# Kernel tuning notes

Measured on AMD Instinct MI355X. Metric: run time of the kernel, lower is better.

## Reference

```python
import jax, jax.numpy as jnp
import numpy as np

N_NODES = 100000

def _spmm(edge_index, edge_weight, support):
    # out[dst] += w * support[src]  == sparse adj @ support
    src, dst = edge_index[0], edge_index[1]
    msgs = support[src] * edge_weight[:, None]
    return jax.ops.segment_sum(msgs, dst, num_segments=N_NODES)


def setup_inputs() -> dict:
    key = jax.random.key(0)
    k1, k2, k3, k4, k5 = jax.random.split(key, 5)
    n_feat, n_hid, n_class = 512, 256, 40
    E = 3200000
    x = jax.random.normal(k1, (N_NODES, n_feat), dtype=jnp.float32)
    edge_index = jax.random.randint(k2, (2, E), 0, N_NODES, dtype=jnp.int64)
    edge_weight = jax.random.uniform(k3, (E,), dtype=jnp.float32)
    # Xavier-uniform-like init
    lim1 = float(np.sqrt(6.0 / (n_feat + n_hid)))
    lim2 = float(np.sqrt(6.0 / (n_hid + n_class)))
    W1 = jax.random.uniform(k4, (n_feat, n_hid), minval=-lim1, maxval=lim1, dtype=jnp.float32)
    W2 = jax.random.uniform(k5, (n_hid, n_class), minval=-lim2, maxval=lim2, dtype=jnp.float32)
    return {"x": x, "edge_index": edge_index, "edge_weight": edge_weight, "W1": W1, "W2": W2}


def reference(x, edge_index, edge_weight, W1, W2):
    # layer 1: dense projection then sparse aggregation, relu
    h = jax.nn.relu(_spmm(edge_index, edge_weight, x @ W1))
    # dropout is identity in eval mode (deterministic reference)
    # layer 2
    logits = _spmm(edge_index, edge_weight, h @ W2)
    return jax.nn.log_softmax(logits, axis=1)
```

## Files before the change

### kernel.cpp

```cpp
#include <hip/hip_runtime.h>
#include <math.h>

#define N_FEAT 512
#define F_HID  256
#define F_OUT  40

#define NBLK1 256
#define CAP   48

typedef unsigned short u16;
typedef unsigned int   u32;
typedef unsigned char  u8;
typedef __attribute__((ext_vector_type(8))) short bf8_t;
typedef __attribute__((ext_vector_type(4))) float f32x4;
typedef __attribute__((ext_vector_type(2))) float f32x2;

__device__ __forceinline__ u16 f2bf(float f) {
    unsigned u = __float_as_uint(f);
    u += 0x7FFFu + ((u >> 16) & 1u);
    return (u16)(u >> 16);
}
__device__ __forceinline__ float bfLo(u32 u) { return __uint_as_float(u << 16); }
__device__ __forceinline__ float bfHi(u32 u) { return __uint_as_float(u & 0xFFFF0000u); }

__global__ void prep_weights(const float* __restrict__ W1, const float* __restrict__ W2,
                             u16* __restrict__ W1T, u16* __restrict__ W2T) {
    int idx = blockIdx.x * blockDim.x + threadIdx.x;
    if (idx < F_HID * N_FEAT) {
        int n = idx >> 9, k = idx & 511;
        W1T[idx] = f2bf(W1[k * F_HID + n]);
    }
    int idx2 = idx - F_HID * N_FEAT;
    if (idx2 >= 0 && idx2 < 48 * 256) {
        int n = idx2 >> 8, k = idx2 & 255;
        W2T[idx2] = (n < F_OUT) ? f2bf(W2[k * F_OUT + n]) : (u16)0;
    }
}

__global__ __launch_bounds__(256) void bucket_kernel(const int* __restrict__ src,
                                                     const int* __restrict__ dst,
                                                     const float* __restrict__ w,
                                                     int2* __restrict__ region,
                                                     int* __restrict__ cnt_g,
                                                     int E, int NB) {
    __shared__ int cnt[1024];
    int tid = threadIdx.x;
    for (int i = tid; i < 1024; i += 256) cnt[i] = 0;
    __syncthreads();
    int2* myreg = region + (size_t)blockIdx.x * NB * CAP;
    for (int i = blockIdx.x * 256 + tid; i < E; i += NBLK1 * 256) {
        int d = dst[i];
        int b = d >> 7;
        int pos = atomicAdd(&cnt[b], 1);
        if (pos < CAP)
            myreg[(size_t)b * CAP + pos] =
                make_int2((d & 127) | (src[i] << 7), __float_as_int(w[i]));
    }
    __syncthreads();
    for (int t = tid; t < NB; t += 256)
        cnt_g[blockIdx.x * NB + t] = min(cnt[t], CAP);
}

__global__ __launch_bounds__(256) void scan_tot(const int* __restrict__ cnt_g,
                                                int* __restrict__ tot, int NB) {
    __shared__ int s[256];
    int b = blockIdx.x, tid = threadIdx.x;
    s[tid] = cnt_g[tid * NB + b];
    __syncthreads();
    for (int d = 128; d > 0; d >>= 1) {
        if (tid < d) s[tid] += s[tid + d];
        __syncthreads();
    }
    if (tid == 0) tot[b] = s[0];
}

__global__ __launch_bounds__(256) void bucket_scan(const int* __restrict__ tot,
                                                   int* __restrict__ Bb, int NB) {
    __shared__ int t4[1024];
    __shared__ int part[256];
    int tid = threadIdx.x;
    for (int i = tid; i < 1024; i += 256) t4[i] = (i < NB) ? tot[i] : 0;
    __syncthreads();
    int loc[4], s = 0;
#pragma unroll
    for (int j = 0; j < 4; ++j) { loc[j] = s; s += t4[tid * 4 + j]; }
    part[tid] = s;
    __syncthreads();
    for (int d = 1; d < 256; d <<= 1) {
        int v = (tid >= d) ? part[tid - d] : 0;
        __syncthreads();
        part[tid] += v;
        __syncthreads();
    }
    int pb = part[tid] - s;
#pragma unroll
    for (int j = 0; j < 4; ++j) {
        int b = tid * 4 + j;
        if (b < NB) Bb[b] = pb + loc[j];
    }
}

__global__ __launch_bounds__(256) void build_csr(const int2* __restrict__ region,
                                                 const int* __restrict__ cnt_g,
                                                 const int* __restrict__ Bb,
                                                 int* __restrict__ deg,
                                                 int* __restrict__ offs,
                                                 int2* __restrict__ edges,
                                                 int M, int NB) {
    int b = blockIdx.x, tid = threadIdx.x;
    __shared__ int hist[128], curi[128], pc[NBLK1], s1[256];
    if (tid < 128) hist[tid] = 0;
    pc[tid] = cnt_g[tid * NB + b];
    __syncthreads();
    int sub = tid >> 4, l = tid & 15;
    for (int bl = sub; bl < NBLK1; bl += 16) {
        int n = pc[bl];
        const int2* rp = region + ((size_t)bl * NB + b) * CAP;
        for (int j = l; j < n; j += 16)
            atomicAdd(&hist[rp[j].x & 127], 1);
    }
    __syncthreads();
    int h = (tid < 128) ? hist[tid] : 0;
    s1[tid] = h;
    __syncthreads();
    for (int dd = 1; dd < 128; dd <<= 1) {
        int v = (tid >= dd) ? s1[tid - dd] : 0;
        __syncthreads();
        s1[tid] += v;
        __syncthreads();
    }
    int base = Bb[b];
    if (tid < 128) {
        int ex = s1[tid] - h;
        curi[tid] = ex;
        int d = b * 128 + tid;
        if (d < M) { deg[d] = h; offs[d] = base + ex; }
    }
    __syncthreads();
    for (int bl = sub; bl < NBLK1; bl += 16) {
        int n = pc[bl];
        const int2* rp = region + ((size_t)bl * NB + b) * CAP;
        for (int j = l; j < n; j += 16) {
            int2 e = rp[j];
            int p = atomicAdd(&curi[e.x & 127], 1);
            edges[base + p] = make_int2(e.x >> 7, e.y);
        }
    }
}

__global__ __launch_bounds__(256) void gemm1_kernel(const float* __restrict__ X,
                                                    const u16* __restrict__ W1T,
                                                    u8* __restrict__ H0, int M) {
    __shared__ float As[2][2048];
    int tid  = threadIdx.x;
    int wv   = tid >> 6, lane = tid & 63;
    int l15  = lane & 15, quad = lane >> 4;
    int m0   = blockIdx.x * 64;

    int p16_0 = wv * 64 + lane;
    int p16_1 = 256 + wv * 64 + lane;
    int r0 = p16_0 >> 3, sc0 = (p16_0 & 7) ^ (r0 & 7);
    int r1 = p16_1 >> 3, sc1 = (p16_1 & 7) ^ (r1 & 7);
    const float* src0 = X + (size_t)min(m0 + r0, M - 1) * N_FEAT + sc0 * 4;
    const float* src1 = X + (size_t)min(m0 + r1, M - 1) * N_FEAT + sc1 * 4;

    f32x4 acc[4][4] = {};

    auto stage = [&](int c, int buf) {
        __builtin_amdgcn_global_load_lds(
            (const __attribute__((address_space(1))) void*)(src0 + c * 32),
            (__attribute__((address_space(3))) void*)(&As[buf][wv * 256]), 16, 0, 0);
        __builtin_amdgcn_global_load_lds(
            (const __attribute__((address_space(1))) void*)(src1 + c * 32),
            (__attribute__((address_space(3))) void*)(&As[buf][1024 + wv * 256]), 16, 0, 0);
    };

    stage(0, 0);
    __syncthreads();
    for (int c = 0; c < 16; ++c) {
        int cur = c & 1;
        if (c + 1 < 16) stage(c + 1, cur ^ 1);
        bf8_t b[4];
#pragma unroll
        for (int nt = 0; nt < 4; ++nt)
            b[nt] = *(const bf8_t*)(W1T + (size_t)(wv * 64 + nt * 16 + l15) * N_FEAT + c * 32 + quad * 8);
#pragma unroll
        for (int mt = 0; mt < 4; ++mt) {
            int m = mt * 16 + l15;
            int scA = (quad * 2) ^ (m & 7);
            int scB = (quad * 2 + 1) ^ (m & 7);
            f32x4 x0 = *(const f32x4*)(&As[cur][m * 32 + scA * 4]);
            f32x4 x1 = *(const f32x4*)(&As[cur][m * 32 + scB * 4]);
            bf8_t a;
            a[0] = (short)f2bf(x0[0]); a[1] = (short)f2bf(x0[1]);
            a[2] = (short)f2bf(x0[2]); a[3] = (short)f2bf(x0[3]);
            a[4] = (short)f2bf(x1[0]); a[5] = (short)f2bf(x1[1]);
            a[6] = (short)f2bf(x1[2]); a[7] = (short)f2bf(x1[3]);
#pragma unroll
            for (int nt = 0; nt < 4; ++nt)
                acc[mt][nt] = __builtin_amdgcn_mfma_f32_16x16x32_bf16(a, b[nt], acc[mt][nt], 0, 0, 0);
        }
        __syncthreads();
    }
#pragma unroll
    for (int mt = 0; mt < 4; ++mt)
#pragma unroll
        for (int nt = 0; nt < 4; ++nt)
#pragma unroll
            for (int r = 0; r < 4; ++r) {
                int row = m0 + mt * 16 + quad * 4 + r;
                if (row < M) {
                    int pk = __builtin_amdgcn_cvt_pk_fp8_f32(acc[mt][nt][r], 0.f, 0, false);
                    H0[(size_t)row * F_HID + wv * 64 + nt * 16 + l15] = (u8)(pk & 0xFF);
                }
            }
}

__global__ __launch_bounds__(256) void spmm1_kernel(const u8* __restrict__ H0,
                                                    const int* __restrict__ offs,
                                                    const int* __restrict__ deg,
                                                    const int2* __restrict__ edges,
                                                    u16* __restrict__ H1, int M) {
    __shared__ int2 sE[4][64];
    int wv = threadIdx.x >> 6, lane = threadIdx.x & 63;
    int d = blockIdx.x * 4 + wv;
    if (d >= M) return;
    int start = offs[d], cnt = deg[d];
    int q = lane >> 4, l16 = lane & 15;
    const u8* hp = H0 + l16 * 16;
    float acc[16] = {};
    for (int base = 0; base < cnt; base += 64) {
        int c = min(64, cnt - base);
        int2 ev = make_int2(0, 0);
        if (lane < c) ev = edges[start + base + lane];
        sE[wv][lane] = ev;
        int jt = (c + 31) >> 5;
        for (int j = 0; j < jt; ++j) {
            int2 e[8];
#pragma unroll
            for (int k = 0; k < 8; ++k)
                e[k] = sE[wv][32 * j + 4 * k + q];
            uint4 v[8];
#pragma unroll
            for (int k = 0; k < 8; ++k)
                v[k] = *(const uint4*)(hp + (size_t)e[k].x * F_HID);
#pragma unroll
            for (int k = 0; k < 8; ++k) {
                if (32 * j + 4 * k < c) {
                    float w = __int_as_float(e[k].y);
                    u32 wd[4] = {v[k].x, v[k].y, v[k].z, v[k].w};
#pragma unroll
                    for (int t = 0; t < 4; ++t) {
                        f32x2 lo = __builtin_amdgcn_cvt_pk_f32_fp8((int)wd[t], false);
                        f32x2 hi = __builtin_amdgcn_cvt_pk_f32_fp8((int)wd[t], true);
                        acc[4 * t + 0] = fmaf(w, lo[0], acc[4 * t + 0]);
                        acc[4 * t + 1] = fmaf(w, lo[1], acc[4 * t + 1]);
                        acc[4 * t + 2] = fmaf(w, hi[0], acc[4 * t + 2]);
                        acc[4 * t + 3] = fmaf(w, hi[1], acc[4 * t + 3]);
                    }
                }
            }
        }
    }
#pragma unroll
    for (int t = 0; t < 16; ++t) {
        acc[t] += __shfl_xor(acc[t], 16);
        acc[t] += __shfl_xor(acc[t], 32);
    }
    if (q == 0) {
        u16 o[16];
#pragma unroll
        for (int t = 0; t < 16; ++t) o[t] = f2bf(fmaxf(acc[t], 0.f));
        uint4 r0, r1;
        r0.x = (u32)o[0]  | ((u32)o[1]  << 16);
        r0.y = (u32)o[2]  | ((u32)o[3]  << 16);
        r0.z = (u32)o[4]  | ((u32)o[5]  << 16);
        r0.w = (u32)o[6]  | ((u32)o[7]  << 16);
        r1.x = (u32)o[8]  | ((u32)o[9]  << 16);
        r1.y = (u32)o[10] | ((u32)o[11] << 16);
        r1.z = (u32)o[12] | ((u32)o[13] << 16);
        r1.w = (u32)o[14] | ((u32)o[15] << 16);
        uint4* dst16 = (uint4*)(H1 + (size_t)d * F_HID + l16 * 16);
        dst16[0] = r0;
        dst16[1] = r1;
    }
}

__global__ __launch_bounds__(256) void gemm2_kernel(const u16* __restrict__ H1,
                                                    const u16* __restrict__ W2T,
                                                    u8* __restrict__ P, int M) {
    __shared__ u16 Bs[2][8192];
    int tid  = threadIdx.x;
    int wv   = tid >> 6, lane = tid & 63;
    int l15  = lane & 15, quad = lane >> 4;
    int m0   = blockIdx.x * 128;

    f32x4 acc[2][3] = {};

    auto stage = [&](int c, int buf) {
#pragma unroll
        for (int jj = 0; jj < 4; ++jj) {
            int p16 = jj * 256 + wv * 64 + lane;
            int r   = p16 >> 3;
            int sc  = (p16 & 7) ^ (r & 7);
            const u16* src = H1 + (size_t)min(m0 + r, M - 1) * F_HID + c * 64 + sc * 8;
            __builtin_amdgcn_global_load_lds(
                (const __attribute__((address_space(1))) void*)src,
                (__attribute__((address_space(3))) void*)(&Bs[buf][jj * 2048 + wv * 512]), 16, 0, 0);
        }
    };

    stage(0, 0);
    __syncthreads();
    for (int c = 0; c < 4; ++c) {
        int cur = c & 1;
        if (c + 1 < 4) stage(c + 1, cur ^ 1);
#pragma unroll
        for (int ks = 0; ks < 2; ++ks) {
            bf8_t b[3];
#pragma unroll
            for (int nt = 0; nt < 3; ++nt)
                b[nt] = *(const bf8_t*)(W2T + (size_t)(nt * 16 + l15) * F_HID + c * 64 + ks * 32 + quad * 8);
#pragma unroll
            for (int mt = 0; mt < 2; ++mt) {
                int m  = wv * 32 + mt * 16 + l15;
                int sc = (ks * 4 + quad) ^ (m & 7);
                bf8_t a = *(const bf8_t*)(&Bs[cur][m * 64 + sc * 8]);
#pragma unroll
                for (int nt = 0; nt < 3; ++nt)
                    acc[mt][nt] = __builtin_amdgcn_mfma_f32_16x16x32_bf16(a, b[nt], acc[mt][nt], 0, 0, 0);
            }
        }
        __syncthreads();
    }
#pragma unroll
    for (int mt = 0; mt < 2; ++mt)
#pragma unroll
        for (int nt = 0; nt < 3; ++nt)
#pragma unroll
            for (int r = 0; r < 4; ++r) {
                int row = m0 + wv * 32 + mt * 16 + quad * 4 + r;
                int col = nt * 16 + l15;
                if (row < M) {
                    u8 val = 0;
                    if (col < F_OUT) {
                        int pk = __builtin_amdgcn_cvt_pk_fp8_f32(acc[mt][nt][r], 0.f, 0, false);
                        val = (u8)(pk & 0xFF);
                    }
                    P[(size_t)row * 64 + col] = val;
                }
            }
    for (int rr = tid; rr < 128; rr += 256) {
        int row = m0 + rr;
        if (row < M) *(uint4*)(P + (size_t)row * 64 + 48) = make_uint4(0, 0, 0, 0);
    }
}

__global__ __launch_bounds__(256) void spmm2_kernel(const u8* __restrict__ P,
                                                    const int* __restrict__ offs,
                                                    const int* __restrict__ deg,
                                                    const int2* __restrict__ edges,
                                                    float* __restrict__ out, int M) {
    __shared__ int2 sE[4][64];
    int wv = threadIdx.x >> 6, lane = threadIdx.x & 63;
    int d = blockIdx.x * 4 + wv;
    if (d >= M) return;
    int start = offs[d], cnt = deg[d];
    int g = lane >> 3, l8 = lane & 7;
    const u8* pp = P + l8 * 8;
    float acc[8] = {};
    for (int base = 0; base < cnt; base += 64) {
        int c = min(64, cnt - base);
        int2 ev = make_int2(0, 0);
        if (lane < c) ev = edges[start + base + lane];
        sE[wv][lane] = ev;
        int2 e[8];
#pragma unroll
        for (int k = 0; k < 8; ++k)
            e[k] = sE[wv][8 * k + g];
        uint2 v[8];
#pragma unroll
        for (int k = 0; k < 8; ++k)
            v[k] = *(const uint2*)(pp + (size_t)e[k].x * 64);
#pragma unroll
        for (int k = 0; k < 8; ++k) {
            if (8 * k < c) {
                float w = __int_as_float(e[k].y);
                f32x2 lo0 = __builtin_amdgcn_cvt_pk_f32_fp8((int)v[k].x, false);
                f32x2 hi0 = __builtin_amdgcn_cvt_pk_f32_fp8((int)v[k].x, true);
                f32x2 lo1 = __builtin_amdgcn_cvt_pk_f32_fp8((int)v[k].y, false);
                f32x2 hi1 = __builtin_amdgcn_cvt_pk_f32_fp8((int)v[k].y, true);
                acc[0] = fmaf(w, lo0[0], acc[0]); acc[1] = fmaf(w, lo0[1], acc[1]);
                acc[2] = fmaf(w, hi0[0], acc[2]); acc[3] = fmaf(w, hi0[1], acc[3]);
                acc[4] = fmaf(w, lo1[0], acc[4]); acc[5] = fmaf(w, lo1[1], acc[5]);
                acc[6] = fmaf(w, hi1[0], acc[6]); acc[7] = fmaf(w, hi1[1], acc[7]);
            }
        }
    }
#pragma unroll
    for (int t = 0; t < 8; ++t) {
        acc[t] += __shfl_xor(acc[t], 8);
        acc[t] += __shfl_xor(acc[t], 16);
        acc[t] += __shfl_xor(acc[t], 32);
    }
    float mx = -INFINITY;
    if (l8 < 5) {
#pragma unroll
        for (int t = 0; t < 8; ++t) mx = fmaxf(mx, acc[t]);
    }
#pragma unroll
    for (int off = 4; off >= 1; off >>= 1) mx = fmaxf(mx, __shfl_xor(mx, off));
    float sm = 0.f;
    if (l8 < 5) {
#pragma unroll
        for (int t = 0; t < 8; ++t) sm += expf(acc[t] - mx);
    }
#pragma unroll
    for (int off = 4; off >= 1; off >>= 1) sm += __shfl_xor(sm, off);
    if (g == 0 && l8 < 5) {
        float lse = mx + logf(sm);
        f32x4 o0, o1;
#pragma unroll
        for (int t = 0; t < 4; ++t) { o0[t] = acc[t] - lse; o1[t] = acc[4 + t] - lse; }
        f32x4* op = (f32x4*)(out + (size_t)d * F_OUT + l8 * 8);
        op[0] = o0;
        op[1] = o1;
    }
}

extern "C" void kernel_launch(void* const* d_in, const int* in_sizes, int n_in,
                              void* d_out, int out_size, void* d_ws, size_t ws_size,
                              hipStream_t stream) {
    const float* x   = (const float*)d_in[0];
    const int*   eix = (const int*)d_in[1];
    const float* ewt = (const float*)d_in[2];
    const float* W1  = (const float*)d_in[3];
    const float* W2  = (const float*)d_in[4];
    float* out = (float*)d_out;

    const int E = in_sizes[2];
    const int M = out_size / F_OUT;
    const int NB = (M + 127) >> 7;
    const int* src = eix;
    const int* dst = eix + E;

    char* ws = (char*)d_ws;
    size_t off = 0;
    auto take = [&](size_t bytes) -> void* {
        void* p = ws + off;
        off = (off + bytes + 255) & ~(size_t)255;
        return p;
    };
    u8*    H0     = (u8*)take((size_t)M * F_HID * sizeof(u8));
    u16*   H1     = (u16*)take((size_t)M * F_HID * sizeof(u16));
    u16*   W1T    = (u16*)take((size_t)F_HID * N_FEAT * sizeof(u16));
    u16*   W2T    = (u16*)take((size_t)48 * 256 * sizeof(u16));
    u8*    P      = (u8*)take((size_t)M * 64 * sizeof(u8));
    int*   deg    = (int*)take((size_t)M * sizeof(int));
    int*   offs   = (int*)take((size_t)M * sizeof(int));
    int*   Bb     = (int*)take(1024 * sizeof(int));
    int*   tot    = (int*)take(1024 * sizeof(int));
    int*   cnt_g  = (int*)take((size_t)NBLK1 * NB * sizeof(int));
    int2*  edges  = (int2*)take((size_t)E * sizeof(int2));
    int2*  region = (int2*)take((size_t)NBLK1 * NB * CAP * sizeof(int2));
    (void)ws_size; (void)n_in;

    int prep_n = F_HID * N_FEAT + 48 * 256;
    prep_weights<<<(prep_n + 255) / 256, 256, 0, stream>>>(W1, W2, W1T, W2T);

    bucket_kernel<<<NBLK1, 256, 0, stream>>>(src, dst, ewt, region, cnt_g, E, NB);
    scan_tot<<<NB, 256, 0, stream>>>(cnt_g, tot, NB);
    bucket_scan<<<1, 256, 0, stream>>>(tot, Bb, NB);
    build_csr<<<NB, 256, 0, stream>>>(region, cnt_g, Bb, deg, offs, edges, M, NB);

    gemm1_kernel<<<(M + 63) / 64, 256, 0, stream>>>(x, W1T, H0, M);
    spmm1_kernel<<<(M + 3) / 4, 256, 0, stream>>>(H0, offs, deg, edges, H1, M);
    gemm2_kernel<<<(M + 127) / 128, 256, 0, stream>>>(H1, W2T, P, M);
    spmm2_kernel<<<(M + 3) / 4, 256, 0, stream>>>(P, offs, deg, edges, out, M);
}
```

Measured before the change: 656.2 us.

## Stage bucketed edges in LDS for CSR build and compact logits rows

build_csr now computes per-source-block offsets with a prefix scan and copies each bucket's edges into a 48KB LDS buffer during the histogram pass. The scatter pass then reads from LDS instead of re-reading the region array from global memory. Separately, the fp8 projected matrix P is stored with a 40-byte row stride instead of 64, which drops the zero-padding stores and shrinks the gather footprint in spmm2. Risks: the large LDS buffer lowers occupancy, any bucket with more than 6144 edges would silently lose edges, and 40-byte rows can straddle cache lines.

```diff
diff --git a/kernel.cpp b/kernel.cpp
--- a/kernel.cpp
+++ b/kernel.cpp
@@ -7,6 +7,7 @@
 
 #define NBLK1 256
 #define CAP   48
+#define SECAP 6144
 
 typedef unsigned short u16;
 typedef unsigned int   u32;
@@ -108,16 +109,31 @@
                                                  int2* __restrict__ edges,
                                                  int M, int NB) {
     int b = blockIdx.x, tid = threadIdx.x;
-    __shared__ int hist[128], curi[128], pc[NBLK1], s1[256];
+    __shared__ int hist[128], curi[128], pc[NBLK1], pco[NBLK1], s1[256];
+    __shared__ int2 sEd[SECAP];
     if (tid < 128) hist[tid] = 0;
-    pc[tid] = cnt_g[tid * NB + b];
-    __syncthreads();
+    int n0 = cnt_g[tid * NB + b];
+    pc[tid] = n0;
+    s1[tid] = n0;
+    __syncthreads();
+    for (int d = 1; d < 256; d <<= 1) {
+        int v = (tid >= d) ? s1[tid - d] : 0;
+        __syncthreads();
+        s1[tid] += v;
+        __syncthreads();
+    }
+    pco[tid] = s1[tid] - n0;
+    __syncthreads();
+    int tot = s1[255];
     int sub = tid >> 4, l = tid & 15;
     for (int bl = sub; bl < NBLK1; bl += 16) {
-        int n = pc[bl];
+        int n = pc[bl], o = pco[bl];
         const int2* rp = region + ((size_t)bl * NB + b) * CAP;
-        for (int j = l; j < n; j += 16)
-            atomicAdd(&hist[rp[j].x & 127], 1);
+        for (int j = l; j < n; j += 16) {
+            int2 e = rp[j];
+            if (o + j < SECAP) sEd[o + j] = e;
+            atomicAdd(&hist[e.x & 127], 1);
+        }
     }
     __syncthreads();
     int h = (tid < 128) ? hist[tid] : 0;
@@ -137,14 +153,11 @@
         if (d < M) { deg[d] = h; offs[d] = base + ex; }
     }
     __syncthreads();
-    for (int bl = sub; bl < NBLK1; bl += 16) {
-        int n = pc[bl];
-        const int2* rp = region + ((size_t)bl * NB + b) * CAP;
-        for (int j = l; j < n; j += 16) {
-            int2 e = rp[j];
-            int p = atomicAdd(&curi[e.x & 127], 1);
-            edges[base + p] = make_int2(e.x >> 7, e.y);
-        }
+    if (tot > SECAP) tot = SECAP;
+    for (int j = tid; j < tot; j += 256) {
+        int2 e = sEd[j];
+        int p = atomicAdd(&curi[e.x & 127], 1);
+        edges[base + p] = make_int2(e.x >> 7, e.y);
     }
 }
 
@@ -341,19 +354,11 @@
             for (int r = 0; r < 4; ++r) {
                 int row = m0 + wv * 32 + mt * 16 + quad * 4 + r;
                 int col = nt * 16 + l15;
-                if (row < M) {
-                    u8 val = 0;
-                    if (col < F_OUT) {
-                        int pk = __builtin_amdgcn_cvt_pk_fp8_f32(acc[mt][nt][r], 0.f, 0, false);
-                        val = (u8)(pk & 0xFF);
-                    }
-                    P[(size_t)row * 64 + col] = val;
+                if (row < M && col < F_OUT) {
+                    int pk = __builtin_amdgcn_cvt_pk_fp8_f32(acc[mt][nt][r], 0.f, 0, false);
+                    P[(size_t)row * 40 + col] = (u8)(pk & 0xFF);
                 }
             }
-    for (int rr = tid; rr < 128; rr += 256) {
-        int row = m0 + rr;
-        if (row < M) *(uint4*)(P + (size_t)row * 64 + 48) = make_uint4(0, 0, 0, 0);
-    }
 }
 
 __global__ __launch_bounds__(256) void spmm2_kernel(const u8* __restrict__ P,
@@ -381,7 +386,7 @@
         uint2 v[8];
 #pragma unroll
         for (int k = 0; k < 8; ++k)
-            v[k] = *(const uint2*)(pp + (size_t)e[k].x * 64);
+            v[k] = *(const uint2*)(pp + (size_t)e[k].x * 40);
 #pragma unroll
         for (int k = 0; k < 8; ++k) {
             if (8 * k < c) {
@@ -455,7 +460,7 @@
     u16*   H1     = (u16*)take((size_t)M * F_HID * sizeof(u16));
     u16*   W1T    = (u16*)take((size_t)F_HID * N_FEAT * sizeof(u16));
     u16*   W2T    = (u16*)take((size_t)48 * 256 * sizeof(u16));
-    u8*    P      = (u8*)take((size_t)M * 64 * sizeof(u8));
+    u8*    P      = (u8*)take((size_t)M * 40 + 256);
     int*   deg    = (int*)take((size_t)M * sizeof(int));
     int*   offs   = (int*)take((size_t)M * sizeof(int));
     int*   Bb     = (int*)take(1024 * sizeof(int));
```

After: 663.6 us. Within noise of the previous version (+1.1%).
